# Performance work log

Hardware: AMD Instinct MI355X
Metric: run time of the kernel (lower is better)

Reference implementation:

```python
import jax, jax.numpy as jnp
import numpy as np

N_NODES = 50000
N_EDGES = 800000
IN_DIM = 96
HID_DIM = 96


def setup_inputs() -> dict:
    key = jax.random.key(0)
    ks = jax.random.split(key, 8)
    inputs = jax.random.normal(ks[0], (N_NODES, IN_DIM), dtype=jnp.float32)
    factor = jax.random.uniform(ks[1], (N_EDGES, 1), dtype=jnp.float32)
    src = jax.random.randint(ks[2], (N_EDGES,), 0, N_NODES, dtype=jnp.int32)
    dst = jax.random.randint(ks[3], (N_EDGES,), 0, N_NODES, dtype=jnp.int32)
    # Linear params (torch nn.Linear: y = x @ W.T + b), uniform(-1/sqrt(fan_in), ..)
    s1 = 1.0 / np.sqrt(IN_DIM)
    s2 = 1.0 / np.sqrt(HID_DIM)
    W1 = jax.random.uniform(ks[4], (HID_DIM, IN_DIM), minval=-s1, maxval=s1, dtype=jnp.float32)
    b1 = jax.random.uniform(ks[5], (HID_DIM,), minval=-s1, maxval=s1, dtype=jnp.float32)
    W2 = jax.random.uniform(ks[6], (IN_DIM, HID_DIM), minval=-s2, maxval=s2, dtype=jnp.float32)
    b2 = jax.random.uniform(ks[7], (IN_DIM,), minval=-s2, maxval=s2, dtype=jnp.float32)
    return {"inputs": inputs, "W1": W1, "b1": b1, "W2": W2, "b2": b2,
            "factor": factor, "src": src, "dst": dst}


def _propagate(feat, factor, src, dst, n_nodes):
    # message = h[src] * edge_factor ; reduce = sum at dst
    msg = feat[src] * factor                       # [E, D]
    return jax.ops.segment_sum(msg, dst, num_segments=n_nodes)


def reference(inputs, W1, b1, W2, b2, factor, src, dst):
    n = inputs.shape[0]
    # in-degree norm: deg^{-1/2}, clamped at 1
    deg = jax.ops.segment_sum(jnp.ones((src.shape[0],), inputs.dtype), dst,
                              num_segments=n)
    norm = jnp.maximum(deg, 1.0) ** -0.5           # [N]
    norm = norm[:, None]                           # [N, 1]

    feat = (inputs @ W1.T + b1) * norm             # [N, H]
    h = jnp.tanh(_propagate(feat, factor, src, dst, n))

    feat = (h @ W2.T + b2) * norm                  # [N, D]
    h = jnp.tanh(_propagate(feat, factor, src, dst, n))

    # dgl.mean_nodes over a single graph -> [1, D]; unsqueeze(-1) -> [1, D, 1]
    pooled = jnp.mean(h, axis=0, keepdims=True)[..., None]
    return jnp.tanh(pooled)
```

## Files before the change

kernel.cpp:

```cpp
#include <hip/hip_runtime.h>
#include <math.h>
#include <type_traits>

#define N_NODES 50000
#define N_EDGES 800000
#define DIM 96
#define BCH 12
#define SCAN_BLK 256
#define NBLK ((N_NODES + SCAN_BLK - 1) / SCAN_BLK)
#define NPB 21
#define NBG ((N_NODES + NPB - 1) / NPB)
#define CAP 768
#define R1_ROWS 24
#define R1_BLOCKS ((NBG + R1_ROWS - 1) / R1_ROWS)

typedef short v8s __attribute__((ext_vector_type(8)));
typedef float v4f __attribute__((ext_vector_type(4)));

__device__ __forceinline__ unsigned short f2bf(float f) {
    unsigned int u = __float_as_uint(f);
    u += 0x7FFFu + ((u >> 16) & 1u);
    return (unsigned short)(u >> 16);
}
__device__ __forceinline__ unsigned int pack2bf(float lo, float hi) {
    return (unsigned int)f2bf(lo) | ((unsigned int)f2bf(hi) << 16);
}
__device__ __forceinline__ float bflo(unsigned int u) { return __uint_as_float(u << 16); }
__device__ __forceinline__ float bfhi(unsigned int u) { return __uint_as_float(u & 0xFFFF0000u); }

__device__ __forceinline__ float fast_tanh(float x) {
    float ax = fabsf(x);
    float t = __expf(-2.0f * ax);
    float r = (1.0f - t) / (1.0f + t);
    return copysignf(r, x);
}

__device__ __forceinline__ void acc8(float* a, uint4 v, float f) {
    a[0] += bflo(v.x) * f; a[1] += bfhi(v.x) * f;
    a[2] += bflo(v.y) * f; a[3] += bfhi(v.y) * f;
    a[4] += bflo(v.z) * f; a[5] += bfhi(v.z) * f;
    a[6] += bflo(v.w) * f; a[7] += bfhi(v.w) * f;
}

union U4S8 { uint4 u; v8s s; };


__global__ void link_edges(const int* __restrict__ dst, int* __restrict__ head,
                           int* __restrict__ nxt) {
    int e = blockIdx.x * blockDim.x + threadIdx.x;
    if (e >= N_EDGES) return;
    int old = atomicExch(&head[dst[e]], e);
    nxt[e] = old;
}

__global__ void walk_count_partials(const int* __restrict__ head, const int* __restrict__ nxt,
                                    int* __restrict__ deg, float* __restrict__ norm,
                                    int* __restrict__ partials) {
    int b = blockIdx.x, t = threadIdx.x;
    int n = b * SCAN_BLK + t;
    int cnt = 0;
    if (n < N_NODES) {
        int p = head[n];
        while (p >= 0) { ++cnt; p = nxt[p]; }
        deg[n] = cnt;
        norm[n] = rsqrtf(fmaxf((float)cnt, 1.0f));
    }
    int v = cnt;
#pragma unroll
    for (int off = 32; off > 0; off >>= 1) v += __shfl_down(v, off, 64);
    __shared__ int ws[4];
    if ((t & 63) == 0) ws[t >> 6] = v;
    __syncthreads();
    if (t == 0) partials[b] = ws[0] + ws[1] + ws[2] + ws[3];
}

__global__ void scan_partials(const int* __restrict__ partials, int* __restrict__ pprefix) {
    __shared__ int sm[SCAN_BLK];
    int t = threadIdx.x;
    int v = (t < NBLK) ? partials[t] : 0;
    sm[t] = v;
    __syncthreads();
    for (int off = 1; off < SCAN_BLK; off <<= 1) {
        int u = (t >= off) ? sm[t - off] : 0;
        __syncthreads();
        sm[t] += u;
        __syncthreads();
    }
    if (t < NBLK) pprefix[t] = sm[t] - v;
}

__global__ void scan_compact(const int* __restrict__ deg, const int* __restrict__ pprefix,
                             const int* __restrict__ head, const int* __restrict__ nxt,
                             const int* __restrict__ src, const float* __restrict__ factor,
                             int* __restrict__ offs, int2* __restrict__ entries) {
    __shared__ int sm[SCAN_BLK];
    int b = blockIdx.x, t = threadIdx.x;
    int idx = b * SCAN_BLK + t;
    int v = (idx < N_NODES) ? deg[idx] : 0;
    sm[t] = v;
    __syncthreads();
    for (int off = 1; off < SCAN_BLK; off <<= 1) {
        int u = (t >= off) ? sm[t - off] : 0;
        __syncthreads();
        sm[t] += u;
        __syncthreads();
    }
    if (idx < N_NODES) {
        int o = pprefix[b] + sm[t] - v;
        offs[idx] = o;
        int p = head[idx];
        while (p >= 0) {
            entries[o++] = make_int2(src[p], __float_as_int(factor[p]));
            p = nxt[p];
        }
    }
    if (b == 0 && t == 0) offs[N_NODES] = N_EDGES;
}


__global__ void swizzle_W(const float* __restrict__ W, uint4* __restrict__ bsw) {
    int idx = blockIdx.x * blockDim.x + threadIdx.x;
    if (idx >= 18 * 64) return;
    int t = idx >> 6, lane = idx & 63;
    int kt = t / 6, jt = t % 6;
    int quad = lane >> 4, l16 = lane & 15;
    const float4* wp = (const float4*)(W + (size_t)(jt * 16 + l16) * DIM + kt * 32 + quad * 8);
    float4 w0 = wp[0], w1 = wp[1];
    bsw[idx] = make_uint4(pack2bf(w0.x, w0.y), pack2bf(w0.z, w0.w),
                          pack2bf(w1.x, w1.y), pack2bf(w1.z, w1.w));
}


#define TILE_SH 104

template <typename T>
__global__ __launch_bounds__(256) void gemm_mfma(const T* __restrict__ X,
                                                 const uint4* __restrict__ bsw,
                                                 const float* __restrict__ bias,
                                                 const float* __restrict__ norm,
                                                 unsigned short* __restrict__ out) {
    __shared__ unsigned short tile[4][16 * TILE_SH];
    int tid = threadIdx.x;
    int wave = tid >> 6, lane = tid & 63;
    int quad = lane >> 4, l16 = lane & 15;
    int n0 = blockIdx.x * 64 + wave * 16;
    int rowc = min(n0 + l16, N_NODES - 1);

    uint4 bfr[18];
#pragma unroll
    for (int t = 0; t < 18; ++t) bfr[t] = bsw[t * 64 + lane];

    v4f acc[6];
#pragma unroll
    for (int jt = 0; jt < 6; ++jt) acc[jt] = (v4f)(0.0f);

#pragma unroll
    for (int kt = 0; kt < 3; ++kt) {
        U4S8 a;
        if constexpr (std::is_same_v<T, float>) {
            const float4* xp = (const float4*)(X + (size_t)rowc * DIM + kt * 32 + quad * 8);
            float4 x0 = xp[0], x1 = xp[1];
            a.u = make_uint4(pack2bf(x0.x, x0.y), pack2bf(x0.z, x0.w),
                             pack2bf(x1.x, x1.y), pack2bf(x1.z, x1.w));
        } else {
            a.u = *(const uint4*)(X + (size_t)rowc * DIM + kt * 32 + quad * 8);
        }
#pragma unroll
        for (int jt = 0; jt < 6; ++jt) {
            U4S8 bb; bb.u = bfr[kt * 6 + jt];
            acc[jt] = __builtin_amdgcn_mfma_f32_16x16x32_bf16(a.s, bb.s, acc[jt], 0, 0, 0);
        }
    }

    float nm[4];
#pragma unroll
    for (int r = 0; r < 4; ++r) nm[r] = norm[min(n0 + quad * 4 + r, N_NODES - 1)];
#pragma unroll
    for (int jt = 0; jt < 6; ++jt) {
        float bj = bias[jt * 16 + l16];
#pragma unroll
        for (int r = 0; r < 4; ++r) {
            float v = (acc[jt][r] + bj) * nm[r];
            tile[wave][(quad * 4 + r) * TILE_SH + jt * 16 + l16] = f2bf(v);
        }
    }
    __builtin_amdgcn_s_waitcnt(0);
#pragma unroll
    for (int i = 0; i < 3; ++i) {
        int chunk = lane + 64 * i;
        int rr = chunk / 12, cc = chunk - rr * 12;
        int gn = n0 + rr;
        if (gn < N_NODES) {
            uint4 v = *(uint4*)&tile[wave][rr * TILE_SH + cc * 8];
            *(uint4*)(out + (size_t)gn * DIM + cc * 8) = v;
        }
    }
}


template <bool DO_TANH, bool POOL>
__global__ void gather_agg_bf16(const unsigned short* __restrict__ feat,
                                const int* __restrict__ offs,
                                const int2* __restrict__ entries,
                                unsigned short* __restrict__ out,
                                float* __restrict__ partials) {
    __shared__ int2 ents[CAP];
    __shared__ float pool[DIM];
    __shared__ int sh_base, sh_cnt;
    int tid = threadIdx.x;
    int n0 = blockIdx.x * NPB;
    int n1 = min(n0 + NPB, N_NODES);
    if (POOL && tid < DIM) pool[tid] = 0.f;
    if (tid == 0) { sh_base = offs[n0]; sh_cnt = offs[n1] - sh_base; }
    __syncthreads();
    int base = sh_base, cnt = sh_cnt;

    int nl = tid / BCH;
    int c  = tid - nl * BCH;
    int n  = n0 + nl;
    bool active = (tid < NPB * BCH) && (n < N_NODES);
    int lb = 0, le = 0;
    if (active) { lb = offs[n] - base; le = offs[n + 1] - base; }

    float a0[8], a1[8];
#pragma unroll
    for (int i = 0; i < 8; ++i) { a0[i] = 0.f; a1[i] = 0.f; }

    for (int tb = 0; tb < cnt; tb += CAP) {
        int tcnt = min(cnt - tb, CAP);
        if (tb) __syncthreads();
        for (int i = tid; i < tcnt; i += 256) ents[i] = entries[base + tb + i];
        __syncthreads();
        int s = max(lb - tb, 0), e = min(le - tb, tcnt);
        int p = s;
        for (; p + 3 < e; p += 4) {
            int2 e0 = ents[p], e1 = ents[p + 1], e2 = ents[p + 2], e3 = ents[p + 3];
            uint4 v0 = *((const uint4*)(feat + (size_t)e0.x * DIM) + c);
            uint4 v1 = *((const uint4*)(feat + (size_t)e1.x * DIM) + c);
            uint4 v2 = *((const uint4*)(feat + (size_t)e2.x * DIM) + c);
            uint4 v3 = *((const uint4*)(feat + (size_t)e3.x * DIM) + c);
            acc8(a0, v0, __int_as_float(e0.y));
            acc8(a1, v1, __int_as_float(e1.y));
            acc8(a0, v2, __int_as_float(e2.y));
            acc8(a1, v3, __int_as_float(e3.y));
        }
        for (; p < e; ++p) {
            int2 e0 = ents[p];
            uint4 v0 = *((const uint4*)(feat + (size_t)e0.x * DIM) + c);
            acc8(a0, v0, __int_as_float(e0.y));
        }
    }

#pragma unroll
    for (int i = 0; i < 8; ++i) a0[i] += a1[i];
    if (DO_TANH || POOL) {
#pragma unroll
        for (int i = 0; i < 8; ++i) a0[i] = fast_tanh(a0[i]);
    }
    if (!POOL) {
        if (active) {
            uint4 o;
            o.x = pack2bf(a0[0], a0[1]);
            o.y = pack2bf(a0[2], a0[3]);
            o.z = pack2bf(a0[4], a0[5]);
            o.w = pack2bf(a0[6], a0[7]);
            ((uint4*)out)[n * BCH + c] = o;
        }
    } else {
        if (active) {
#pragma unroll
            for (int i = 0; i < 8; ++i) atomicAdd(&pool[c * 8 + i], a0[i]);
        }
        __syncthreads();
        if (tid < DIM) partials[(size_t)blockIdx.x * DIM + tid] = pool[tid];
    }
}


__global__ void reduce_stage1(const float* __restrict__ poolpart, float* __restrict__ stage1) {
    __shared__ float pool[DIM];
    int b = blockIdx.x, t = threadIdx.x;
    if (t < DIM) pool[t] = 0.f;
    __syncthreads();
    const int base = b * R1_ROWS * DIM;
    float loc = 0.f;
    int lastc = -1;
    for (int i = t; i < R1_ROWS * DIM; i += 256) {
        int gi = base + i;
        if (gi < NBG * DIM) {
            int col = i % DIM;
            if (col != lastc) {
                if (lastc >= 0) atomicAdd(&pool[lastc], loc);
                lastc = col; loc = 0.f;
            }
            loc += poolpart[gi];
        }
    }
    if (lastc >= 0) atomicAdd(&pool[lastc], loc);
    __syncthreads();
    if (t < DIM) stage1[b * DIM + t] = pool[t];
}

__global__ void reduce_stage2(const float* __restrict__ stage1, float* __restrict__ out) {
    __shared__ float sm[960];
    int t = threadIdx.x;
    int col = t % DIM, slice = t / DIM;
    float s = 0.f;
    for (int k = slice; k < R1_BLOCKS; k += 10) s += stage1[k * DIM + col];
    sm[t] = s;
    __syncthreads();
    if (t < DIM) {
        float tot = 0.f;
#pragma unroll
        for (int i = 0; i < 10; ++i) tot += sm[i * DIM + t];
        out[t] = tanhf(tot * (1.0f / N_NODES));
    }
}


extern "C" void kernel_launch(void* const* d_in, const int* in_sizes, int n_in,
                              void* d_out, int out_size, void* d_ws, size_t ws_size,
                              hipStream_t stream) {
    const float* inputs = (const float*)d_in[0];
    const float* W1     = (const float*)d_in[1];
    const float* b1     = (const float*)d_in[2];
    const float* W2     = (const float*)d_in[3];
    const float* b2     = (const float*)d_in[4];
    const float* factor = (const float*)d_in[5];
    const int*   src    = (const int*)d_in[6];
    const int*   dst    = (const int*)d_in[7];
    float* out = (float*)d_out;

    char* ws = (char*)d_ws;
    int*            head     = (int*)(ws + 0);
    int*            nxt      = (int*)(ws + 262144);
    int*            deg      = (int*)(ws + 3670016);
    int*            offs     = (int*)(ws + 3932160);
    float*          norm     = (float*)(ws + 4194304);
    int*            partials = (int*)(ws + 4456448);
    int*            pprefix  = (int*)(ws + 4458496);
    int2*           entries  = (int2*)(ws + 4718592);
    unsigned short* bufA     = (unsigned short*)(ws + 11534336);
    unsigned short* bufB     = (unsigned short*)(ws + 21364736);
    float*          poolpart = (float*)(ws + 31195136);
    float*          stage1   = (float*)(ws + 32145536);
    uint4*          bsw1     = (uint4*)(ws + 33554432);
    uint4*          bsw2     = (uint4*)(ws + 33574912);

    swizzle_W<<<5, 256, 0, stream>>>(W1, bsw1);
    swizzle_W<<<5, 256, 0, stream>>>(W2, bsw2);

    hipMemsetAsync(head, 0xFF, N_NODES * sizeof(int), stream);
    link_edges<<<(N_EDGES + 255) / 256, 256, 0, stream>>>(dst, head, nxt);
    walk_count_partials<<<NBLK, SCAN_BLK, 0, stream>>>(head, nxt, deg, norm, partials);
    scan_partials<<<1, SCAN_BLK, 0, stream>>>(partials, pprefix);
    scan_compact<<<NBLK, SCAN_BLK, 0, stream>>>(deg, pprefix, head, nxt, src, factor,
                                                offs, entries);

    const int GEMM_BLOCKS = (N_NODES + 63) / 64;

    gemm_mfma<float><<<GEMM_BLOCKS, 256, 0, stream>>>(inputs, bsw1, b1, norm, bufA);
    gather_agg_bf16<true, false><<<NBG, 256, 0, stream>>>(bufA, offs, entries, bufB, nullptr);

    gemm_mfma<unsigned short><<<GEMM_BLOCKS, 256, 0, stream>>>(bufB, bsw2, b2, norm, bufA);
    gather_agg_bf16<false, true><<<NBG, 256, 0, stream>>>(bufA, offs, entries, nullptr, poolpart);

    reduce_stage1<<<R1_BLOCKS, 256, 0, stream>>>(poolpart, stage1);
    reduce_stage2<<<1, 960, 0, stream>>>(stage1, out);
}
```

Before: 263.0 us.

## Build CSR via atomic degree count and scatter instead of linked-list walks

Result: slower. 271.2 us (+3.1%).

```diff
diff --git a/kernel.cpp b/kernel.cpp
--- a/kernel.cpp
+++ b/kernel.cpp
@@ -45,33 +45,27 @@
 union U4S8 { uint4 u; v8s s; };
 
 
-__global__ void link_edges(const int* __restrict__ dst, int* __restrict__ head,
-                           int* __restrict__ nxt) {
+__global__ void count_deg(const int* __restrict__ dst, int* __restrict__ deg) {
     int e = blockIdx.x * blockDim.x + threadIdx.x;
-    if (e >= N_EDGES) return;
-    int old = atomicExch(&head[dst[e]], e);
-    nxt[e] = old;
-}
-
-__global__ void walk_count_partials(const int* __restrict__ head, const int* __restrict__ nxt,
-                                    int* __restrict__ deg, float* __restrict__ norm,
-                                    int* __restrict__ partials) {
+    if (e < N_EDGES) atomicAdd(&deg[dst[e]], 1);
+}
+
+__global__ void deg_partials(const int* __restrict__ deg, float* __restrict__ norm,
+                             int* __restrict__ partials) {
     int b = blockIdx.x, t = threadIdx.x;
     int n = b * SCAN_BLK + t;
-    int cnt = 0;
+    int v = 0;
     if (n < N_NODES) {
-        int p = head[n];
-        while (p >= 0) { ++cnt; p = nxt[p]; }
-        deg[n] = cnt;
-        norm[n] = rsqrtf(fmaxf((float)cnt, 1.0f));
-    }
-    int v = cnt;
-#pragma unroll
-    for (int off = 32; off > 0; off >>= 1) v += __shfl_down(v, off, 64);
-    __shared__ int ws[4];
-    if ((t & 63) == 0) ws[t >> 6] = v;
-    __syncthreads();
-    if (t == 0) partials[b] = ws[0] + ws[1] + ws[2] + ws[3];
+        v = deg[n];
+        norm[n] = rsqrtf(fmaxf((float)v, 1.0f));
+    }
+    int s = v;
+#pragma unroll
+    for (int off = 32; off > 0; off >>= 1) s += __shfl_down(s, off, 64);
+    __shared__ int ws_[4];
+    if ((t & 63) == 0) ws_[t >> 6] = s;
+    __syncthreads();
+    if (t == 0) partials[b] = ws_[0] + ws_[1] + ws_[2] + ws_[3];
 }
 
 __global__ void scan_partials(const int* __restrict__ partials, int* __restrict__ pprefix) {
@@ -89,10 +83,8 @@
     if (t < NBLK) pprefix[t] = sm[t] - v;
 }
 
-__global__ void scan_compact(const int* __restrict__ deg, const int* __restrict__ pprefix,
-                             const int* __restrict__ head, const int* __restrict__ nxt,
-                             const int* __restrict__ src, const float* __restrict__ factor,
-                             int* __restrict__ offs, int2* __restrict__ entries) {
+__global__ void make_offsets(const int* __restrict__ deg, const int* __restrict__ pprefix,
+                             int* __restrict__ offs, int* __restrict__ cursor) {
     __shared__ int sm[SCAN_BLK];
     int b = blockIdx.x, t = threadIdx.x;
     int idx = b * SCAN_BLK + t;
@@ -108,13 +100,19 @@
     if (idx < N_NODES) {
         int o = pprefix[b] + sm[t] - v;
         offs[idx] = o;
-        int p = head[idx];
-        while (p >= 0) {
-            entries[o++] = make_int2(src[p], __float_as_int(factor[p]));
-            p = nxt[p];
-        }
+        cursor[idx] = o;
     }
     if (b == 0 && t == 0) offs[N_NODES] = N_EDGES;
+}
+
+__global__ void scatter_edges(const int* __restrict__ src, const int* __restrict__ dst,
+                              const float* __restrict__ factor, int* __restrict__ cursor,
+                              int2* __restrict__ entries) {
+    int e = blockIdx.x * blockDim.x + threadIdx.x;
+    if (e >= N_EDGES) return;
+    int d = dst[e];
+    int pos = atomicAdd(&cursor[d], 1);
+    entries[pos] = make_int2(src[e], __float_as_int(factor[e]));
 }
 
 
@@ -233,21 +231,41 @@
         __syncthreads();
         int s = max(lb - tb, 0), e = min(le - tb, tcnt);
         int p = s;
+        for (; p + 7 < e; p += 8) {
+            int2 q0 = ents[p + 0], q1 = ents[p + 1], q2 = ents[p + 2], q3 = ents[p + 3];
+            int2 q4 = ents[p + 4], q5 = ents[p + 5], q6 = ents[p + 6], q7 = ents[p + 7];
+            uint4 v0 = *((const uint4*)(feat + (size_t)q0.x * DIM) + c);
+            uint4 v1 = *((const uint4*)(feat + (size_t)q1.x * DIM) + c);
+            uint4 v2 = *((const uint4*)(feat + (size_t)q2.x * DIM) + c);
+            uint4 v3 = *((const uint4*)(feat + (size_t)q3.x * DIM) + c);
+            uint4 v4 = *((const uint4*)(feat + (size_t)q4.x * DIM) + c);
+            uint4 v5 = *((const uint4*)(feat + (size_t)q5.x * DIM) + c);
+            uint4 v6 = *((const uint4*)(feat + (size_t)q6.x * DIM) + c);
+            uint4 v7 = *((const uint4*)(feat + (size_t)q7.x * DIM) + c);
+            acc8(a0, v0, __int_as_float(q0.y));
+            acc8(a1, v1, __int_as_float(q1.y));
+            acc8(a0, v2, __int_as_float(q2.y));
+            acc8(a1, v3, __int_as_float(q3.y));
+            acc8(a0, v4, __int_as_float(q4.y));
+            acc8(a1, v5, __int_as_float(q5.y));
+            acc8(a0, v6, __int_as_float(q6.y));
+            acc8(a1, v7, __int_as_float(q7.y));
+        }
         for (; p + 3 < e; p += 4) {
-            int2 e0 = ents[p], e1 = ents[p + 1], e2 = ents[p + 2], e3 = ents[p + 3];
-            uint4 v0 = *((const uint4*)(feat + (size_t)e0.x * DIM) + c);
-            uint4 v1 = *((const uint4*)(feat + (size_t)e1.x * DIM) + c);
-            uint4 v2 = *((const uint4*)(feat + (size_t)e2.x * DIM) + c);
-            uint4 v3 = *((const uint4*)(feat + (size_t)e3.x * DIM) + c);
-            acc8(a0, v0, __int_as_float(e0.y));
-            acc8(a1, v1, __int_as_float(e1.y));
-            acc8(a0, v2, __int_as_float(e2.y));
-            acc8(a1, v3, __int_as_float(e3.y));
+            int2 q0 = ents[p], q1 = ents[p + 1], q2 = ents[p + 2], q3 = ents[p + 3];
+            uint4 v0 = *((const uint4*)(feat + (size_t)q0.x * DIM) + c);
+            uint4 v1 = *((const uint4*)(feat + (size_t)q1.x * DIM) + c);
+            uint4 v2 = *((const uint4*)(feat + (size_t)q2.x * DIM) + c);
+            uint4 v3 = *((const uint4*)(feat + (size_t)q3.x * DIM) + c);
+            acc8(a0, v0, __int_as_float(q0.y));
+            acc8(a1, v1, __int_as_float(q1.y));
+            acc8(a0, v2, __int_as_float(q2.y));
+            acc8(a1, v3, __int_as_float(q3.y));
         }
         for (; p < e; ++p) {
-            int2 e0 = ents[p];
-            uint4 v0 = *((const uint4*)(feat + (size_t)e0.x * DIM) + c);
-            acc8(a0, v0, __int_as_float(e0.y));
+            int2 q0 = ents[p];
+            uint4 v0 = *((const uint4*)(feat + (size_t)q0.x * DIM) + c);
+            acc8(a0, v0, __int_as_float(q0.y));
         }
     }
 
@@ -332,9 +350,8 @@
     float* out = (float*)d_out;
 
     char* ws = (char*)d_ws;
-    int*            head     = (int*)(ws + 0);
-    int*            nxt      = (int*)(ws + 262144);
-    int*            deg      = (int*)(ws + 3670016);
+    int*            deg      = (int*)(ws + 0);
+    int*            cursor   = (int*)(ws + 262144);
     int*            offs     = (int*)(ws + 3932160);
     float*          norm     = (float*)(ws + 4194304);
     int*            partials = (int*)(ws + 4456448);
@@ -350,12 +367,12 @@
     swizzle_W<<<5, 256, 0, stream>>>(W1, bsw1);
     swizzle_W<<<5, 256, 0, stream>>>(W2, bsw2);
 
-    hipMemsetAsync(head, 0xFF, N_NODES * sizeof(int), stream);
-    link_edges<<<(N_EDGES + 255) / 256, 256, 0, stream>>>(dst, head, nxt);
-    walk_count_partials<<<NBLK, SCAN_BLK, 0, stream>>>(head, nxt, deg, norm, partials);
+    hipMemsetAsync(deg, 0, N_NODES * sizeof(int), stream);
+    count_deg<<<(N_EDGES + 255) / 256, 256, 0, stream>>>(dst, deg);
+    deg_partials<<<NBLK, SCAN_BLK, 0, stream>>>(deg, norm, partials);
     scan_partials<<<1, SCAN_BLK, 0, stream>>>(partials, pprefix);
-    scan_compact<<<NBLK, SCAN_BLK, 0, stream>>>(deg, pprefix, head, nxt, src, factor,
-                                                offs, entries);
+    make_offsets<<<NBLK, SCAN_BLK, 0, stream>>>(deg, pprefix, offs, cursor);
+    scatter_edges<<<(N_EDGES + 255) / 256, 256, 0, stream>>>(src, dst, factor, cursor, entries);
 
     const int GEMM_BLOCKS = (N_NODES + 63) / 64;
 
```
